# Optimization experiments

Measured on AMD Instinct MI355X. Metric: run time of the kernel, lower is better.

The kernel has to match this reference:

```python
import jax, jax.numpy as jnp
import numpy as np

HIDDEN = 2048
NUM_HEADS = 16
HEAD_DIM = 128
BLOCK_SIZE = 64
NUM_ACTIVE_BLOCKS = 4  # diagonal pattern -> bandwidth = 2 blocks each side
NEG_INF = -1e30  # stand-in for -inf that is safe under softmax in fp32


def _block_diagonal_additive_mask(seq_len: int) -> jnp.ndarray:
    """Token-level additive mask [S, S]; 0 where block |bi-bj|<=bandwidth, -inf else."""
    bandwidth = NUM_ACTIVE_BLOCKS // 2
    bid = jnp.arange(seq_len) // BLOCK_SIZE  # [S]
    active = jnp.abs(bid[:, None] - bid[None, :]) <= bandwidth  # [S, S] bool
    return jnp.where(active, 0.0, NEG_INF).astype(jnp.float32)


def setup_inputs() -> dict:
    key = jax.random.key(0)
    k0, k1, k2, k3, k4 = jax.random.split(key, 5)
    B, S = 2, 2048
    scale = 1.0 / np.sqrt(HIDDEN)
    return {
        "hidden_states": jax.random.normal(k0, (B, S, HIDDEN), dtype=jnp.float32),
        "Wq": jax.random.normal(k1, (HIDDEN, NUM_HEADS * HEAD_DIM), dtype=jnp.float32) * scale,
        "Wk": jax.random.normal(k2, (HIDDEN, NUM_HEADS * HEAD_DIM), dtype=jnp.float32) * scale,
        "Wv": jax.random.normal(k3, (HIDDEN, NUM_HEADS * HEAD_DIM), dtype=jnp.float32) * scale,
        "Wo": jax.random.normal(k4, (NUM_HEADS * HEAD_DIM, HIDDEN), dtype=jnp.float32) * scale,
    }


def reference(hidden_states, Wq, Wk, Wv, Wo):
    B, S, _ = hidden_states.shape
    scaling = HEAD_DIM ** -0.5

    # projections -> [B, H, S, D]
    def split_heads(x):
        return x.reshape(B, S, NUM_HEADS, HEAD_DIM).transpose(0, 2, 1, 3)

    q = split_heads(hidden_states @ Wq)
    k = split_heads(hidden_states @ Wk)
    v = split_heads(hidden_states @ Wv)

    mask = _block_diagonal_additive_mask(S)  # [S, S]

    # scores [B, H, S, S]
    scores = jnp.einsum("bhsd,bhtd->bhst", q, k) * scaling + mask[None, None]
    attn = jax.nn.softmax(scores.astype(jnp.float32), axis=-1).astype(q.dtype)

    out = jnp.einsum("bhst,bhtd->bhsd", attn, v)  # [B, H, S, D]
    out = out.transpose(0, 2, 1, 3).reshape(B, S, NUM_HEADS * HEAD_DIM)
    return out @ Wo
```

## Files before the change

### kernel.cpp

```cpp
#include <hip/hip_runtime.h>

typedef __attribute__((ext_vector_type(4))) float f32x4;
typedef __attribute__((ext_vector_type(8))) _Float16 f16x8;
typedef __attribute__((ext_vector_type(4))) _Float16 f16x4;

__device__ __forceinline__ void gload_lds16(const void* g, void* l) {
  __builtin_amdgcn_global_load_lds((__attribute__((address_space(1))) void*)(g),
                                   (__attribute__((address_space(3))) void*)(l), 16, 0, 0);
}

__global__ __launch_bounds__(256) void cast_f32_f16(const float* __restrict__ x,
                                                    _Float16* __restrict__ y, int n) {
  int i = (blockIdx.x * 256 + threadIdx.x) * 4;
  if (i < n) {
    float4 v = *(const float4*)(x + i);
    f16x4 o = { (_Float16)v.x, (_Float16)v.y, (_Float16)v.z, (_Float16)v.w };
    *(f16x4*)(y + i) = o;
  }
}

__global__ __launch_bounds__(256) void wtrans(const float* __restrict__ W0, const float* __restrict__ W1,
                                              const float* __restrict__ W2, const float* __restrict__ W3,
                                              _Float16* __restrict__ out) {
  const float* W = blockIdx.z == 0 ? W0 : blockIdx.z == 1 ? W1 : blockIdx.z == 2 ? W2 : W3;
  _Float16* Wt = out + (size_t)blockIdx.z * (2048u * 2048u);
  __shared__ _Float16 tile[64][65];
  const int tid = threadIdx.x;
  const int k0 = blockIdx.y * 64, n0 = blockIdx.x * 64;
  #pragma unroll
  for (int p = 0; p < 4; ++p) {
    int o = p * 256 + tid, r = o >> 4, c = o & 15;
    float4 v = *(const float4*)(W + (size_t)(k0 + r) * 2048 + n0 + c * 4);
    tile[r][c * 4 + 0] = (_Float16)v.x;
    tile[r][c * 4 + 1] = (_Float16)v.y;
    tile[r][c * 4 + 2] = (_Float16)v.z;
    tile[r][c * 4 + 3] = (_Float16)v.w;
  }
  __syncthreads();
  #pragma unroll
  for (int p = 0; p < 2; ++p) {
    int o = p * 256 + tid, nl = o >> 3, c = o & 7;
    f16x8 u;
    #pragma unroll
    for (int i = 0; i < 8; ++i) u[i] = tile[c * 8 + i][nl];
    *(f16x8*)(Wt + (size_t)(n0 + nl) * 2048 + k0 + c * 8) = u;
  }
}

__global__ __launch_bounds__(256) void vtrans(const _Float16* __restrict__ V, _Float16* __restrict__ Vt) {
  const int s0 = blockIdx.x * 64, d0 = blockIdx.y * 64, bh = blockIdx.z;
  const int b = bh >> 4, h = bh & 15;
  __shared__ _Float16 tile[64][65];
  const int tid = threadIdx.x;
  #pragma unroll
  for (int p = 0; p < 2; ++p) {
    int o = p * 256 + tid, sl = o >> 3, c = o & 7;
    f16x8 v = *(const f16x8*)(V + (size_t)(b * 2048 + s0 + sl) * 2048 + h * 128 + d0 + c * 8);
    #pragma unroll
    for (int i = 0; i < 8; ++i) tile[sl][c * 8 + i] = v[i];
  }
  __syncthreads();
  #pragma unroll
  for (int p = 0; p < 2; ++p) {
    int o = p * 256 + tid, dl = o >> 3, c = o & 7;
    f16x8 u;
    #pragma unroll
    for (int i = 0; i < 8; ++i) u[i] = tile[c * 8 + i][dl];
    *(f16x8*)(Vt + (size_t)(bh * 128 + d0 + dl) * 2048 + s0 + c * 8) = u;
  }
}

template <typename OutT>
__global__ __launch_bounds__(256) void gemm_bt(const _Float16* __restrict__ A,
                                               const _Float16* __restrict__ Bt,
                                               OutT* __restrict__ C,
                                               int K, int N, size_t zsB, size_t zsC) {
  Bt += (size_t)blockIdx.z * zsB;
  C  += (size_t)blockIdx.z * zsC;
  __shared__ _Float16 As[128 * 32];
  __shared__ _Float16 Bs[128 * 32];
  const int tid = threadIdx.x;
  const int m0 = blockIdx.y * 128, n0 = blockIdx.x * 128;
  const int lane = tid & 63, w = tid >> 6, l16 = lane & 15, quad = lane >> 4;
  const int wm = (w & 1) * 64, wn = (w >> 1) * 64;
  f32x4 acc[4][4];
  #pragma unroll
  for (int i = 0; i < 4; ++i)
    #pragma unroll
    for (int j = 0; j < 4; ++j) acc[i][j] = (f32x4){0.f, 0.f, 0.f, 0.f};

  const int r0 = tid >> 2;
  const int c0 = ((tid & 3) ^ ((r0 >> 1) & 3)) * 8;
  const int swz = (quad ^ ((l16 >> 1) & 3)) * 8;

  for (int k0 = 0; k0 < K; k0 += 32) {
    __syncthreads();
    #pragma unroll
    for (int p = 0; p < 2; ++p) {
      int r = p * 64 + r0;
      gload_lds16(A  + (size_t)(m0 + r) * K + k0 + c0, (char*)As + (p * 256 + tid) * 16);
      gload_lds16(Bt + (size_t)(n0 + r) * K + k0 + c0, (char*)Bs + (p * 256 + tid) * 16);
    }
    __builtin_amdgcn_s_waitcnt(0);
    __syncthreads();
    f16x8 af[4], bfv[4];
    #pragma unroll
    for (int i = 0; i < 4; ++i) af[i]  = *(const f16x8*)(As + (wm + i * 16 + l16) * 32 + swz);
    #pragma unroll
    for (int j = 0; j < 4; ++j) bfv[j] = *(const f16x8*)(Bs + (wn + j * 16 + l16) * 32 + swz);
    #pragma unroll
    for (int i = 0; i < 4; ++i)
      #pragma unroll
      for (int j = 0; j < 4; ++j)
        acc[i][j] = __builtin_amdgcn_mfma_f32_16x16x32_f16(bfv[j], af[i], acc[i][j], 0, 0, 0);
  }
  #pragma unroll
  for (int i = 0; i < 4; ++i) {
    const size_t row = (size_t)(m0 + wm + i * 16 + l16);
    #pragma unroll
    for (int j = 0; j < 4; ++j) {
      const int col = n0 + wn + j * 16 + quad * 4;
      if constexpr (sizeof(OutT) == 2) {
        f16x4 o = { (_Float16)acc[i][j][0], (_Float16)acc[i][j][1],
                    (_Float16)acc[i][j][2], (_Float16)acc[i][j][3] };
        *(f16x4*)((_Float16*)C + row * N + col) = o;
      } else {
        *(f32x4*)((float*)C + row * N + col) = acc[i][j];
      }
    }
  }
}

__global__ __launch_bounds__(256) void attn(const _Float16* __restrict__ Qg,
                                            const _Float16* __restrict__ Kg,
                                            const _Float16* __restrict__ Vtg,
                                            _Float16* __restrict__ Og) {
  const int qb = blockIdx.x, h = blockIdx.y, b = blockIdx.z;
  __shared__ _Float16 Qs[64 * 128];
  __shared__ _Float16 Ks[64 * 128];
  __shared__ _Float16 Vs[128 * 64];
  const int tid = threadIdx.x;
  const int lane = tid & 63, w = tid >> 6, l16 = lane & 15, quad = lane >> 4;
  const char* QsB = (const char*)Qs;
  const char* KsB = (const char*)Ks;
  const char* VsB = (const char*)Vs;

  #pragma unroll
  for (int p = 0; p < 4; ++p) {
    int o = p * 256 + tid, r = o >> 4, c = o & 15;
    gload_lds16(Qg + (size_t)(b * 2048 + qb * 64 + r) * 2048 + h * 128 + ((c ^ (r & 15)) * 8),
                (char*)Qs + o * 16);
  }
  __builtin_amdgcn_s_waitcnt(0);
  __syncthreads();
  f16x8 qf[4];
  #pragma unroll
  for (int ks = 0; ks < 4; ++ks)
    qf[ks] = *(const f16x8*)(QsB + (w * 16 + l16) * 256 + (((ks * 4 + quad) ^ l16) * 16));

  f32x4 sc[5][4];
  #pragma unroll
  for (int jj = 0; jj < 5; ++jj) {
    int j = qb - 2 + jj;
    int jc = j < 0 ? 0 : (j > 31 ? 31 : j);
    __syncthreads();
    #pragma unroll
    for (int p = 0; p < 4; ++p) {
      int o = p * 256 + tid, r = o >> 4, c = o & 15;
      gload_lds16(Kg + (size_t)(b * 2048 + jc * 64 + r) * 2048 + h * 128 + ((c ^ (r & 15)) * 8),
                  (char*)Ks + o * 16);
    }
    __builtin_amdgcn_s_waitcnt(0);
    __syncthreads();
    #pragma unroll
    for (int kt = 0; kt < 4; ++kt) {
      f32x4 c4 = {0.f, 0.f, 0.f, 0.f};
      #pragma unroll
      for (int ks = 0; ks < 4; ++ks) {
        f16x8 kf = *(const f16x8*)(KsB + (kt * 16 + l16) * 256 + (((ks * 4 + quad) ^ l16) * 16));
        c4 = __builtin_amdgcn_mfma_f32_16x16x32_f16(kf, qf[ks], c4, 0, 0, 0);
      }
      sc[jj][kt] = c4;
    }
  }

  const float scale = 0.08838834764831845f;
  float rmax = -1e30f;
  #pragma unroll
  for (int jj = 0; jj < 5; ++jj) {
    const int j = qb - 2 + jj;
    const bool valid = (j >= 0) && (j < 32);
    #pragma unroll
    for (int kt = 0; kt < 4; ++kt)
      #pragma unroll
      for (int r = 0; r < 4; ++r) {
        float v = valid ? sc[jj][kt][r] * scale : -1e30f;
        sc[jj][kt][r] = v;
        rmax = fmaxf(rmax, v);
      }
  }
  rmax = fmaxf(rmax, __shfl_xor(rmax, 16));
  rmax = fmaxf(rmax, __shfl_xor(rmax, 32));
  float rsum = 0.f;
  #pragma unroll
  for (int jj = 0; jj < 5; ++jj)
    #pragma unroll
    for (int kt = 0; kt < 4; ++kt)
      #pragma unroll
      for (int r = 0; r < 4; ++r) {
        float p = __expf(sc[jj][kt][r] - rmax);
        sc[jj][kt][r] = p;
        rsum += p;
      }
  rsum += __shfl_xor(rsum, 16);
  rsum += __shfl_xor(rsum, 32);
  const float pinv = 1.0f / rsum;

  f32x4 oacc[8];
  #pragma unroll
  for (int dt = 0; dt < 8; ++dt) oacc[dt] = (f32x4){0.f, 0.f, 0.f, 0.f};
  #pragma unroll
  for (int jj = 0; jj < 5; ++jj) {
    int j = qb - 2 + jj;
    int jc = j < 0 ? 0 : (j > 31 ? 31 : j);
    __syncthreads();
    #pragma unroll
    for (int p = 0; p < 4; ++p) {
      int o = p * 256 + tid, d = o >> 3, c = o & 7;
      gload_lds16(Vtg + (size_t)((b * 16 + h) * 128 + d) * 2048 + jc * 64 + ((c ^ (d & 7)) * 8),
                  (char*)Vs + o * 16);
    }
    __builtin_amdgcn_s_waitcnt(0);
    __syncthreads();
    #pragma unroll
    for (int kt = 0; kt < 4; ++kt) {
      f16x4 pb = { (_Float16)sc[jj][kt][0], (_Float16)sc[jj][kt][1],
                   (_Float16)sc[jj][kt][2], (_Float16)sc[jj][kt][3] };
      #pragma unroll
      for (int dt = 0; dt < 8; ++dt) {
        f16x4 vv = *(const f16x4*)(VsB + (dt * 16 + l16) * 128 +
                                   (((2 * kt + (quad >> 1)) ^ (l16 & 7)) * 16) + (quad & 1) * 8);
        oacc[dt] = __builtin_amdgcn_mfma_f32_16x16x16f16(vv, pb, oacc[dt], 0, 0, 0);
      }
    }
  }
  const size_t orow = (size_t)(b * 2048 + qb * 64 + w * 16 + l16);
  #pragma unroll
  for (int dt = 0; dt < 8; ++dt) {
    f16x4 ov = { (_Float16)(oacc[dt][0] * pinv), (_Float16)(oacc[dt][1] * pinv),
                 (_Float16)(oacc[dt][2] * pinv), (_Float16)(oacc[dt][3] * pinv) };
    *(f16x4*)(Og + orow * 2048 + h * 128 + dt * 16 + quad * 4) = ov;
  }
}

extern "C" void kernel_launch(void* const* d_in, const int* in_sizes, int n_in,
                              void* d_out, int out_size, void* d_ws, size_t ws_size,
                              hipStream_t stream) {
  const float* Hs = (const float*)d_in[0];
  const float* Wq = (const float*)d_in[1];
  const float* Wk = (const float*)d_in[2];
  const float* Wv = (const float*)d_in[3];
  const float* Wo = (const float*)d_in[4];
  _Float16* Hb  = (_Float16*)d_ws;
  _Float16* Wt  = Hb  + 8388608;
  _Float16* Qb  = Wt  + 16777216;
  _Float16* Kb  = Qb  + 8388608;
  _Float16* Vb  = Kb  + 8388608;
  _Float16* Vtb = Vb  + 8388608;
  _Float16* Ob  = Vtb + 8388608;
  float* out = (float*)d_out;

  cast_f32_f16<<<8192, 256, 0, stream>>>(Hs, Hb, 8388608);
  wtrans<<<dim3(32, 32, 4), 256, 0, stream>>>(Wq, Wk, Wv, Wo, Wt);
  gemm_bt<_Float16><<<dim3(16, 32, 3), 256, 0, stream>>>(Hb, Wt, Qb, 2048, 2048,
                                                         (size_t)4194304, (size_t)8388608);
  vtrans<<<dim3(32, 2, 32), 256, 0, stream>>>(Vb, Vtb);
  attn<<<dim3(32, 16, 2), 256, 0, stream>>>(Qb, Kb, Vtb, Ob);
  gemm_bt<float><<<dim3(16, 32, 1), 256, 0, stream>>>(Ob, Wt + 3 * 4194304, out, 2048, 2048,
                                                      (size_t)0, (size_t)0);
}
```

Before: 383.1 us.

## Process two query blocks per workgroup with online softmax sharing K/V tiles

The attention kernel now handles 128 query rows per workgroup (two 64-row query blocks, each wave doing 32 rows). It walks 6 key blocks with an online-softmax (running max and sum) so each K and V tile loaded into LDS is reused by both query blocks. K and V loads are merged into a single sync per iteration. This cuts redundant K/V global loads and halves the grid, but waves skip non-overlapping key blocks, which can leave some waves idle, and it adds rescaling work and register pressure.

```diff
diff --git a/kernel.cpp b/kernel.cpp
--- a/kernel.cpp
+++ b/kernel.cpp
@@ -135,34 +135,44 @@
                                             const _Float16* __restrict__ Kg,
                                             const _Float16* __restrict__ Vtg,
                                             _Float16* __restrict__ Og) {
-  const int qb = blockIdx.x, h = blockIdx.y, b = blockIdx.z;
-  __shared__ _Float16 Qs[64 * 128];
+  const int t = blockIdx.x, h = blockIdx.y, b = blockIdx.z;
+  __shared__ _Float16 Qs[128 * 128];
   __shared__ _Float16 Ks[64 * 128];
   __shared__ _Float16 Vs[128 * 64];
   const int tid = threadIdx.x;
   const int lane = tid & 63, w = tid >> 6, l16 = lane & 15, quad = lane >> 4;
+  const int qbw = 2 * t + (w >> 1);
   const char* QsB = (const char*)Qs;
   const char* KsB = (const char*)Ks;
   const char* VsB = (const char*)Vs;
 
   #pragma unroll
-  for (int p = 0; p < 4; ++p) {
+  for (int p = 0; p < 8; ++p) {
     int o = p * 256 + tid, r = o >> 4, c = o & 15;
-    gload_lds16(Qg + (size_t)(b * 2048 + qb * 64 + r) * 2048 + h * 128 + ((c ^ (r & 15)) * 8),
+    gload_lds16(Qg + (size_t)(b * 2048 + t * 128 + r) * 2048 + h * 128 + ((c ^ (r & 15)) * 8),
                 (char*)Qs + o * 16);
   }
   __builtin_amdgcn_s_waitcnt(0);
   __syncthreads();
-  f16x8 qf[4];
-  #pragma unroll
-  for (int ks = 0; ks < 4; ++ks)
-    qf[ks] = *(const f16x8*)(QsB + (w * 16 + l16) * 256 + (((ks * 4 + quad) ^ l16) * 16));
-
-  f32x4 sc[5][4];
-  #pragma unroll
-  for (int jj = 0; jj < 5; ++jj) {
-    int j = qb - 2 + jj;
-    int jc = j < 0 ? 0 : (j > 31 ? 31 : j);
+  f16x8 qf[2][4];
+  #pragma unroll
+  for (int qc = 0; qc < 2; ++qc)
+    #pragma unroll
+    for (int ks = 0; ks < 4; ++ks)
+      qf[qc][ks] = *(const f16x8*)(QsB + (w * 32 + qc * 16 + l16) * 256 +
+                                   (((ks * 4 + quad) ^ l16) * 16));
+
+  const float scale = 0.08838834764831845f;
+  float m_[2] = {-1e30f, -1e30f}, l_[2] = {0.f, 0.f};
+  f32x4 oacc[8][2];
+  #pragma unroll
+  for (int dt = 0; dt < 8; ++dt)
+    #pragma unroll
+    for (int qc = 0; qc < 2; ++qc) oacc[dt][qc] = (f32x4){0.f, 0.f, 0.f, 0.f};
+
+  for (int jj = 0; jj < 6; ++jj) {
+    const int j = 2 * t - 2 + jj;
+    const int jc = j < 0 ? 0 : (j > 31 ? 31 : j);
     __syncthreads();
     #pragma unroll
     for (int p = 0; p < 4; ++p) {
@@ -170,60 +180,6 @@
       gload_lds16(Kg + (size_t)(b * 2048 + jc * 64 + r) * 2048 + h * 128 + ((c ^ (r & 15)) * 8),
                   (char*)Ks + o * 16);
     }
-    __builtin_amdgcn_s_waitcnt(0);
-    __syncthreads();
-    #pragma unroll
-    for (int kt = 0; kt < 4; ++kt) {
-      f32x4 c4 = {0.f, 0.f, 0.f, 0.f};
-      #pragma unroll
-      for (int ks = 0; ks < 4; ++ks) {
-        f16x8 kf = *(const f16x8*)(KsB + (kt * 16 + l16) * 256 + (((ks * 4 + quad) ^ l16) * 16));
-        c4 = __builtin_amdgcn_mfma_f32_16x16x32_f16(kf, qf[ks], c4, 0, 0, 0);
-      }
-      sc[jj][kt] = c4;
-    }
-  }
-
-  const float scale = 0.08838834764831845f;
-  float rmax = -1e30f;
-  #pragma unroll
-  for (int jj = 0; jj < 5; ++jj) {
-    const int j = qb - 2 + jj;
-    const bool valid = (j >= 0) && (j < 32);
-    #pragma unroll
-    for (int kt = 0; kt < 4; ++kt)
-      #pragma unroll
-      for (int r = 0; r < 4; ++r) {
-        float v = valid ? sc[jj][kt][r] * scale : -1e30f;
-        sc[jj][kt][r] = v;
-        rmax = fmaxf(rmax, v);
-      }
-  }
-  rmax = fmaxf(rmax, __shfl_xor(rmax, 16));
-  rmax = fmaxf(rmax, __shfl_xor(rmax, 32));
-  float rsum = 0.f;
-  #pragma unroll
-  for (int jj = 0; jj < 5; ++jj)
-    #pragma unroll
-    for (int kt = 0; kt < 4; ++kt)
-      #pragma unroll
-      for (int r = 0; r < 4; ++r) {
-        float p = __expf(sc[jj][kt][r] - rmax);
-        sc[jj][kt][r] = p;
-        rsum += p;
-      }
-  rsum += __shfl_xor(rsum, 16);
-  rsum += __shfl_xor(rsum, 32);
-  const float pinv = 1.0f / rsum;
-
-  f32x4 oacc[8];
-  #pragma unroll
-  for (int dt = 0; dt < 8; ++dt) oacc[dt] = (f32x4){0.f, 0.f, 0.f, 0.f};
-  #pragma unroll
-  for (int jj = 0; jj < 5; ++jj) {
-    int j = qb - 2 + jj;
-    int jc = j < 0 ? 0 : (j > 31 ? 31 : j);
-    __syncthreads();
     #pragma unroll
     for (int p = 0; p < 4; ++p) {
       int o = p * 256 + tid, d = o >> 3, c = o & 7;
@@ -232,24 +188,83 @@
     }
     __builtin_amdgcn_s_waitcnt(0);
     __syncthreads();
-    #pragma unroll
-    for (int kt = 0; kt < 4; ++kt) {
-      f16x4 pb = { (_Float16)sc[jj][kt][0], (_Float16)sc[jj][kt][1],
-                   (_Float16)sc[jj][kt][2], (_Float16)sc[jj][kt][3] };
-      #pragma unroll
-      for (int dt = 0; dt < 8; ++dt) {
-        f16x4 vv = *(const f16x4*)(VsB + (dt * 16 + l16) * 128 +
-                                   (((2 * kt + (quad >> 1)) ^ (l16 & 7)) * 16) + (quad & 1) * 8);
-        oacc[dt] = __builtin_amdgcn_mfma_f32_16x16x16f16(vv, pb, oacc[dt], 0, 0, 0);
+
+    const bool valid = (j >= 0) && (j <= 31) && (j >= qbw - 2) && (j <= qbw + 2);
+    if (valid) {
+      f32x4 sc[4][2];
+      #pragma unroll
+      for (int kt = 0; kt < 4; ++kt)
+        #pragma unroll
+        for (int qc = 0; qc < 2; ++qc) sc[kt][qc] = (f32x4){0.f, 0.f, 0.f, 0.f};
+      #pragma unroll
+      for (int kt = 0; kt < 4; ++kt)
+        #pragma unroll
+        for (int ks = 0; ks < 4; ++ks) {
+          f16x8 kf = *(const f16x8*)(KsB + (kt * 16 + l16) * 256 + (((ks * 4 + quad) ^ l16) * 16));
+          #pragma unroll
+          for (int qc = 0; qc < 2; ++qc)
+            sc[kt][qc] = __builtin_amdgcn_mfma_f32_16x16x32_f16(kf, qf[qc][ks], sc[kt][qc], 0, 0, 0);
+        }
+      #pragma unroll
+      for (int qc = 0; qc < 2; ++qc) {
+        float mj = -1e30f;
+        #pragma unroll
+        for (int kt = 0; kt < 4; ++kt)
+          #pragma unroll
+          for (int r = 0; r < 4; ++r) {
+            float v = sc[kt][qc][r] * scale;
+            sc[kt][qc][r] = v;
+            mj = fmaxf(mj, v);
+          }
+        mj = fmaxf(mj, __shfl_xor(mj, 16));
+        mj = fmaxf(mj, __shfl_xor(mj, 32));
+        const float mn = fmaxf(m_[qc], mj);
+        const float alpha = __expf(m_[qc] - mn);
+        float s_ = 0.f;
+        #pragma unroll
+        for (int kt = 0; kt < 4; ++kt)
+          #pragma unroll
+          for (int r = 0; r < 4; ++r) {
+            float p = __expf(sc[kt][qc][r] - mn);
+            sc[kt][qc][r] = p;
+            s_ += p;
+          }
+        s_ += __shfl_xor(s_, 16);
+        s_ += __shfl_xor(s_, 32);
+        l_[qc] = l_[qc] * alpha + s_;
+        m_[qc] = mn;
+        #pragma unroll
+        for (int dt = 0; dt < 8; ++dt) oacc[dt][qc] *= alpha;
       }
-    }
-  }
-  const size_t orow = (size_t)(b * 2048 + qb * 64 + w * 16 + l16);
-  #pragma unroll
-  for (int dt = 0; dt < 8; ++dt) {
-    f16x4 ov = { (_Float16)(oacc[dt][0] * pinv), (_Float16)(oacc[dt][1] * pinv),
-                 (_Float16)(oacc[dt][2] * pinv), (_Float16)(oacc[dt][3] * pinv) };
-    *(f16x4*)(Og + orow * 2048 + h * 128 + dt * 16 + quad * 4) = ov;
+      #pragma unroll
+      for (int kt = 0; kt < 4; ++kt) {
+        f16x4 pb[2];
+        #pragma unroll
+        for (int qc = 0; qc < 2; ++qc)
+          pb[qc] = (f16x4){ (_Float16)sc[kt][qc][0], (_Float16)sc[kt][qc][1],
+                            (_Float16)sc[kt][qc][2], (_Float16)sc[kt][qc][3] };
+        #pragma unroll
+        for (int dt = 0; dt < 8; ++dt) {
+          f16x4 vv = *(const f16x4*)(VsB + (dt * 16 + l16) * 128 +
+                                     (((2 * kt + (quad >> 1)) ^ (l16 & 7)) * 16) + (quad & 1) * 8);
+          #pragma unroll
+          for (int qc = 0; qc < 2; ++qc)
+            oacc[dt][qc] = __builtin_amdgcn_mfma_f32_16x16x16f16(vv, pb[qc], oacc[dt][qc], 0, 0, 0);
+        }
+      }
+    }
+  }
+
+  #pragma unroll
+  for (int qc = 0; qc < 2; ++qc) {
+    const float pinv = 1.0f / l_[qc];
+    const size_t orow = (size_t)(b * 2048 + t * 128 + w * 32 + qc * 16 + l16);
+    #pragma unroll
+    for (int dt = 0; dt < 8; ++dt) {
+      f16x4 ov = { (_Float16)(oacc[dt][qc][0] * pinv), (_Float16)(oacc[dt][qc][1] * pinv),
+                   (_Float16)(oacc[dt][qc][2] * pinv), (_Float16)(oacc[dt][qc][3] * pinv) };
+      *(f16x4*)(Og + orow * 2048 + h * 128 + dt * 16 + quad * 4) = ov;
+    }
   }
 }
 
@@ -275,7 +290,7 @@
   gemm_bt<_Float16><<<dim3(16, 32, 3), 256, 0, stream>>>(Hb, Wt, Qb, 2048, 2048,
                                                          (size_t)4194304, (size_t)8388608);
   vtrans<<<dim3(32, 2, 32), 256, 0, stream>>>(Vb, Vtb);
-  attn<<<dim3(32, 16, 2), 256, 0, stream>>>(Qb, Kb, Vtb, Ob);
+  attn<<<dim3(16, 16, 2), 256, 0, stream>>>(Qb, Kb, Vtb, Ob);
   gemm_bt<float><<<dim3(16, 32, 1), 256, 0, stream>>>(Ob, Wt + 3 * 4194304, out, 2048, 2048,
                                                       (size_t)0, (size_t)0);
 }
```

After: 388.3 us. Within noise of the previous version (+1.4%).
